# Performance work log

Measured on AMD Instinct MI355X. Metric: run time of the kernel, lower is better.

## Reference

```python
import jax, jax.numpy as jnp
import numpy as np

LAMBDA_ENERGY = 0.1
LAMBDA_COV = 0.005
TWO_PI = 2.0 * np.pi
EPS = 1e-12


def setup_inputs() -> dict:
    key = jax.random.key(0)
    k1, k2, k3, k4 = jax.random.split(key, 4)
    B, T, C, D, K, F = 32, 1024, 8, 8, 8, 64
    x = jax.random.normal(k1, (B, T, C, F), dtype=jnp.float32)
    x_hat = jax.random.normal(k2, (B, T, C, F), dtype=jnp.float32)
    z = jax.random.normal(k3, (B, T, C, D), dtype=jnp.float32)
    # gamma is a mixture-responsibility tensor (softmax output in DAGMM)
    gamma = jax.nn.softmax(jax.random.uniform(k4, (B, T, C, K), dtype=jnp.float32) * 4.0, axis=-1)
    return {"x": x, "x_hat": x_hat, "z": z, "gamma": gamma}


def _gmm_energy(z, gamma):
    # z: [B,T,C,D], gamma: [B,T,C,K]
    N = gamma.shape[0] * gamma.shape[1] * gamma.shape[2]
    gsum = jnp.sum(gamma, axis=(0, 1, 2))                      # [K]
    phi = gsum / N                                             # [K]
    mu = jnp.einsum('btck,btcd->kd', gamma, z) / gsum[:, None]  # [K,D]
    z_mu = z[..., None, :] - mu                                # [B,T,C,K,D]
    cov = jnp.einsum('btck,btcki,btckj->kij', gamma, z_mu, z_mu) / gsum[:, None, None]  # [K,D,D]

    D = cov.shape[-1]
    cov_k = cov + EPS * jnp.eye(D, dtype=cov.dtype)            # [K,D,D]
    cov_inv = jnp.linalg.inv(cov_k)                            # batched small-matrix inverse
    L = jnp.linalg.cholesky(TWO_PI * cov_k)                    # [K,D,D]
    det_cov = jnp.prod(jnp.diagonal(L, axis1=-2, axis2=-1), axis=-1)  # [K], = sqrt(det(2*pi*cov))
    cov_diag = jnp.sum(1.0 / jnp.diagonal(cov_k, axis1=-2, axis2=-1))

    # quadratic form per sample/component: [B,T,C,K]
    quad = jnp.einsum('btcki,kij,btckj->btck', z_mu, cov_inv, z_mu)
    E = jnp.exp(-0.5 * quad)
    E_z = -jnp.log(jnp.sum(phi * E / jnp.sqrt(det_cov), axis=-1) + EPS)
    return jnp.mean(E_z), cov_diag


def reference(x, x_hat, z, gamma):
    reconst_loss = jnp.mean((x_hat - x) ** 2)
    sample_energy, cov_diag = _gmm_energy(z, gamma)
    return reconst_loss + LAMBDA_ENERGY * sample_energy + LAMBDA_COV * cov_diag
```

## Files before the change

kernel.cpp:

```cpp
#include <hip/hip_runtime.h>
#include <math.h>

#define WS_RED   0
#define WS_EN    2048
#define WS_MU    3072
#define WS_CINV  3136
#define WS_COEF  3648
#define WS_CD    3656
#define WS_STATP 4096

static constexpr int NSAMP = 32 * 1024 * 8;
static constexpr int NX4   = NSAMP * 64 / 4;
static constexpr int RE_BLOCKS   = 2048;
static constexpr int STAT_BLOCKS = 256;
static constexpr int EN_BLOCKS   = 1024;
static constexpr float EPSF = 1e-12f;

__device__ inline float wave_reduce_sum(float v) {
    #pragma unroll
    for (int m = 1; m < 64; m <<= 1) v += __shfl_xor(v, m, 64);
    return v;
}
__device__ inline double wave_reduce_sum_d(double v) {
    #pragma unroll
    for (int m = 1; m < 64; m <<= 1) v += __shfl_xor(v, m, 64);
    return v;
}

__global__ __launch_bounds__(256) void krecon(const float4* __restrict__ x,
                                              const float4* __restrict__ xh,
                                              float* __restrict__ ws) {
    __shared__ float lds[4];
    const int t = blockIdx.x * 256 + threadIdx.x;

    float4 xa[8], xb[8];
    #pragma unroll
    for (int i = 0; i < 8; ++i) xa[i] = x[t + i * (RE_BLOCKS * 256)];
    #pragma unroll
    for (int i = 0; i < 8; ++i) xb[i] = xh[t + i * (RE_BLOCKS * 256)];

    float a0 = 0.f, a1 = 0.f, a2 = 0.f, a3 = 0.f;
    #pragma unroll
    for (int i = 0; i < 8; ++i) {
        float d0 = xb[i].x - xa[i].x;
        float d1 = xb[i].y - xa[i].y;
        float d2 = xb[i].z - xa[i].z;
        float d3 = xb[i].w - xa[i].w;
        a0 = fmaf(d0, d0, a0);
        a1 = fmaf(d1, d1, a1);
        a2 = fmaf(d2, d2, a2);
        a3 = fmaf(d3, d3, a3);
    }
    float acc = (a0 + a1) + (a2 + a3);

    acc = wave_reduce_sum(acc);
    int w = threadIdx.x >> 6;
    if ((threadIdx.x & 63) == 0) lds[w] = acc;
    __syncthreads();
    if (threadIdx.x == 0)
        ws[WS_RED + blockIdx.x] = lds[0] + lds[1] + lds[2] + lds[3];
}

__global__ __launch_bounds__(256) void kstats(const float4* __restrict__ z4,
                                              const float* __restrict__ gamma,
                                              float* __restrict__ ws) {
    __shared__ float lds[4][360];
    float acc[45];
    #pragma unroll
    for (int i = 0; i < 45; ++i) acc[i] = 0.f;

    const int k    = threadIdx.x & 7;
    const int grp  = (blockIdx.x << 5) | (threadIdx.x >> 3);
    constexpr int NGRP  = STAT_BLOCKS << 5;
    constexpr int ITERS = NSAMP / NGRP;

    for (int it = 0; it < ITERS; it += 4) {
        float4 za[4], zb[4];
        float gg[4];
        #pragma unroll
        for (int u = 0; u < 4; ++u) {
            int n = grp + (it + u) * NGRP;
            za[u] = z4[n * 2];
            zb[u] = z4[n * 2 + 1];
            gg[u] = gamma[n * 8 + k];
        }
        #pragma unroll
        for (int u = 0; u < 4; ++u) {
            float zv[8] = {za[u].x, za[u].y, za[u].z, za[u].w,
                           zb[u].x, zb[u].y, zb[u].z, zb[u].w};
            float g = gg[u];
            acc[0] += g;
            float gz[8];
            #pragma unroll
            for (int i = 0; i < 8; ++i) { gz[i] = g * zv[i]; acc[1 + i] += gz[i]; }
            #pragma unroll
            for (int i = 0; i < 8; ++i) {
                #pragma unroll
                for (int j = 0; j < 8; ++j) {
                    if (j <= i)
                        acc[9 + (i * (i + 1)) / 2 + j] =
                            fmaf(gz[i], zv[j], acc[9 + (i * (i + 1)) / 2 + j]);
                }
            }
        }
    }

    #pragma unroll
    for (int i = 0; i < 45; ++i) {
        float v = acc[i];
        v += __shfl_xor(v, 8, 64);
        v += __shfl_xor(v, 16, 64);
        v += __shfl_xor(v, 32, 64);
        acc[i] = v;
    }
    int lane = threadIdx.x & 63, w = threadIdx.x >> 6;
    if (lane < 8) {
        #pragma unroll
        for (int i = 0; i < 45; ++i) lds[w][lane * 45 + i] = acc[i];
    }
    __syncthreads();
    for (int v = threadIdx.x; v < 360; v += 256) {
        ws[WS_STATP + blockIdx.x * 360 + v] =
            lds[0][v] + lds[1][v] + lds[2][v] + lds[3][v];
    }
}

__global__ void kfinalize(float* __restrict__ ws) {
    __shared__ double sstat[360];
    int v = threadIdx.x;
    if (v < 360) {
        const float* p = &ws[WS_STATP + v];
        double s0 = 0.0, s1 = 0.0, s2 = 0.0, s3 = 0.0;
        #pragma unroll 4
        for (int b = 0; b < STAT_BLOCKS; b += 4) {
            s0 += (double)p[(b + 0) * 360];
            s1 += (double)p[(b + 1) * 360];
            s2 += (double)p[(b + 2) * 360];
            s3 += (double)p[(b + 3) * 360];
        }
        sstat[v] = (s0 + s1) + (s2 + s3);
    }
    __syncthreads();

    int k = threadIdx.x;
    if (k < 8) {
        const double* st = &sstat[k * 45];
        double g = st[0];
        double mu[8];
        for (int d = 0; d < 8; ++d) mu[d] = st[1 + d] / g;
        double A[8][8];
        {
            int t = 0;
            for (int i = 0; i < 8; ++i)
                for (int j = 0; j <= i; ++j) {
                    double val = st[9 + t] / g - mu[i] * mu[j];
                    A[i][j] = val; A[j][i] = val; ++t;
                }
        }
        for (int d = 0; d < 8; ++d) A[d][d] += (double)EPSF;

        double cd = 0.0;
        for (int d = 0; d < 8; ++d) cd += 1.0 / A[d][d];
        ws[WS_CD + k] = (float)cd;

        double L[8][8] = {};
        for (int i = 0; i < 8; ++i) {
            for (int j = 0; j <= i; ++j) {
                double s = A[i][j];
                for (int p = 0; p < j; ++p) s -= L[i][p] * L[j][p];
                if (i == j) L[i][i] = sqrt(s);
                else        L[i][j] = s / L[j][j];
            }
        }
        double M[8][8] = {};
        for (int i = 0; i < 8; ++i) {
            M[i][i] = 1.0 / L[i][i];
            for (int j = 0; j < i; ++j) {
                double s = 0.0;
                for (int p = j; p < i; ++p) s -= L[i][p] * M[p][j];
                M[i][j] = s / L[i][i];
            }
        }
        for (int i = 0; i < 8; ++i)
            for (int j = 0; j < 8; ++j) {
                double s = 0.0;
                int p0 = i > j ? i : j;
                for (int p = p0; p < 8; ++p) s += M[p][i] * M[p][j];
                ws[WS_CINV + k * 64 + i * 8 + j] = (float)s;
            }

        double det = 1.0;
        for (int d = 0; d < 8; ++d) det *= L[d][d];
        double c = 2.0 * M_PI;
        det *= c * c * c * c;
        double phi = g / (double)NSAMP;
        ws[WS_COEF + k] = (float)(phi / sqrt(det));
        for (int d = 0; d < 8; ++d) ws[WS_MU + k * 8 + d] = (float)mu[d];
    }
}

__global__ __launch_bounds__(256, 4) void kenergy(const float4* __restrict__ z4,
                                                  float* __restrict__ ws) {
    __shared__ float smu[64], scinv[512], scoef[8];
    __shared__ float lds[4];
    for (int i = threadIdx.x; i < 64; i += 256) smu[i] = ws[WS_MU + i];
    for (int i = threadIdx.x; i < 512; i += 256) scinv[i] = ws[WS_CINV + i];
    if (threadIdx.x < 8) scoef[threadIdx.x] = ws[WS_COEF + threadIdx.x];
    __syncthreads();

    const int n = blockIdx.x * 256 + threadIdx.x;
    float4 a = z4[n * 2], b = z4[n * 2 + 1];
    float zv[8] = {a.x, a.y, a.z, a.w, b.x, b.y, b.z, b.w};
    float sacc = 0.f;

    #pragma unroll 1
    for (int k = 0; k < 8; ++k) {
        float dv[8];
        #pragma unroll
        for (int i = 0; i < 8; ++i) dv[i] = zv[i] - smu[k * 8 + i];
        float quad = 0.f;
        #pragma unroll
        for (int i = 0; i < 8; ++i) {
            float4 c0 = *(const float4*)&scinv[k * 64 + i * 8];
            float4 c1 = *(const float4*)&scinv[k * 64 + i * 8 + 4];
            float r;
            r = c0.x * dv[0];
            r = fmaf(c0.y, dv[1], r);
            r = fmaf(c0.z, dv[2], r);
            r = fmaf(c0.w, dv[3], r);
            r = fmaf(c1.x, dv[4], r);
            r = fmaf(c1.y, dv[5], r);
            r = fmaf(c1.z, dv[6], r);
            r = fmaf(c1.w, dv[7], r);
            quad = fmaf(dv[i], r, quad);
        }
        sacc = fmaf(scoef[k], __expf(-0.5f * quad), sacc);
    }

    float acc = -__logf(sacc + EPSF);

    acc = wave_reduce_sum(acc);
    int w = threadIdx.x >> 6;
    if ((threadIdx.x & 63) == 0) lds[w] = acc;
    __syncthreads();
    if (threadIdx.x == 0)
        ws[WS_EN + blockIdx.x] = lds[0] + lds[1] + lds[2] + lds[3];
}

__global__ void kfinal(const float* __restrict__ ws, float* __restrict__ out) {
    __shared__ double ldsR[4], ldsE[4];
    double accR = 0.0, accE = 0.0;
    #pragma unroll 4
    for (int i = threadIdx.x; i < RE_BLOCKS; i += 256) accR += (double)ws[WS_RED + i];
    #pragma unroll 4
    for (int i = threadIdx.x; i < EN_BLOCKS; i += 256) accE += (double)ws[WS_EN + i];
    accR = wave_reduce_sum_d(accR);
    accE = wave_reduce_sum_d(accE);
    int w = threadIdx.x >> 6;
    if ((threadIdx.x & 63) == 0) { ldsR[w] = accR; ldsE[w] = accE; }
    __syncthreads();
    if (threadIdx.x == 0) {
        double R = ldsR[0] + ldsR[1] + ldsR[2] + ldsR[3];
        double E = ldsE[0] + ldsE[1] + ldsE[2] + ldsE[3];
        double cd = 0.0;
        for (int k = 0; k < 8; ++k) cd += (double)ws[WS_CD + k];
        double loss = R / ((double)NSAMP * 64.0)
                    + 0.1 * (E / (double)NSAMP)
                    + 0.005 * cd;
        out[0] = (float)loss;
    }
}

extern "C" void kernel_launch(void* const* d_in, const int* in_sizes, int n_in,
                              void* d_out, int out_size, void* d_ws, size_t ws_size,
                              hipStream_t stream) {
    const float* x     = (const float*)d_in[0];
    const float* xh    = (const float*)d_in[1];
    const float* z     = (const float*)d_in[2];
    const float* gamma = (const float*)d_in[3];
    float* ws = (float*)d_ws;

    krecon<<<RE_BLOCKS, 256, 0, stream>>>((const float4*)x, (const float4*)xh, ws);
    kstats<<<STAT_BLOCKS, 256, 0, stream>>>((const float4*)z, gamma, ws);
    kfinalize<<<1, 512, 0, stream>>>(ws);
    kenergy<<<EN_BLOCKS, 256, 0, stream>>>((const float4*)z, ws);
    kfinal<<<1, 256, 0, stream>>>(ws, (float*)d_out);
}
```

Before: 199.8 us.

## Fuse all stages into one persistent kernel with software grid barriers

Replaces the five kernel launches with a single persistent kernel of 1024 blocks that uses atomic-counter grid barriers to sequence reconstruction/stats, GMM parameter finalization, energy, and the final reduction. The reconstruction work is rebalanced so that the stats blocks take a smaller slice and the other blocks take more, which lets the stats pass overlap with the bandwidth-heavy reconstruction. The intent is to remove launch gaps and idle tails between stages. In exchange it relies on all 1024 blocks being co-resident (4 blocks per CU at 256 threads), adds spin-wait barrier cost and a memset, and leaves most of the grid idle while block 0 finalizes.

```diff
diff --git a/kernel.cpp b/kernel.cpp
--- a/kernel.cpp
+++ b/kernel.cpp
@@ -1,19 +1,20 @@
 #include <hip/hip_runtime.h>
 #include <math.h>
 
-#define WS_RED   0
-#define WS_EN    2048
-#define WS_MU    3072
-#define WS_CINV  3136
-#define WS_COEF  3648
-#define WS_CD    3656
+#define TPB   256
+#define GRID  1024
+#define SBLK  256
+
+#define WS_RED   64
+#define WS_EN    1088
+#define WS_MU    2112
+#define WS_CINV  2176
+#define WS_COEF  2688
+#define WS_CD    2696
 #define WS_STATP 4096
 
-static constexpr int NSAMP = 32 * 1024 * 8;
-static constexpr int NX4   = NSAMP * 64 / 4;
-static constexpr int RE_BLOCKS   = 2048;
-static constexpr int STAT_BLOCKS = 256;
-static constexpr int EN_BLOCKS   = 1024;
+static constexpr int NSAMP = 262144;
+static constexpr int NX4   = 4194304;
 static constexpr float EPSF = 1e-12f;
 
 __device__ inline float wave_reduce_sum(float v) {
@@ -27,247 +28,266 @@
     return v;
 }
 
-__global__ __launch_bounds__(256) void krecon(const float4* __restrict__ x,
-                                              const float4* __restrict__ xh,
-                                              float* __restrict__ ws) {
-    __shared__ float lds[4];
-    const int t = blockIdx.x * 256 + threadIdx.x;
-
-    float4 xa[8], xb[8];
-    #pragma unroll
-    for (int i = 0; i < 8; ++i) xa[i] = x[t + i * (RE_BLOCKS * 256)];
-    #pragma unroll
-    for (int i = 0; i < 8; ++i) xb[i] = xh[t + i * (RE_BLOCKS * 256)];
-
-    float a0 = 0.f, a1 = 0.f, a2 = 0.f, a3 = 0.f;
-    #pragma unroll
-    for (int i = 0; i < 8; ++i) {
-        float d0 = xb[i].x - xa[i].x;
-        float d1 = xb[i].y - xa[i].y;
-        float d2 = xb[i].z - xa[i].z;
-        float d3 = xb[i].w - xa[i].w;
-        a0 = fmaf(d0, d0, a0);
-        a1 = fmaf(d1, d1, a1);
-        a2 = fmaf(d2, d2, a2);
-        a3 = fmaf(d3, d3, a3);
-    }
-    float acc = (a0 + a1) + (a2 + a3);
-
-    acc = wave_reduce_sum(acc);
-    int w = threadIdx.x >> 6;
-    if ((threadIdx.x & 63) == 0) lds[w] = acc;
+__device__ inline void grid_barrier(unsigned* cnt, unsigned target) {
     __syncthreads();
-    if (threadIdx.x == 0)
-        ws[WS_RED + blockIdx.x] = lds[0] + lds[1] + lds[2] + lds[3];
-}
-
-__global__ __launch_bounds__(256) void kstats(const float4* __restrict__ z4,
-                                              const float* __restrict__ gamma,
-                                              float* __restrict__ ws) {
-    __shared__ float lds[4][360];
-    float acc[45];
-    #pragma unroll
-    for (int i = 0; i < 45; ++i) acc[i] = 0.f;
-
-    const int k    = threadIdx.x & 7;
-    const int grp  = (blockIdx.x << 5) | (threadIdx.x >> 3);
-    constexpr int NGRP  = STAT_BLOCKS << 5;
-    constexpr int ITERS = NSAMP / NGRP;
-
-    for (int it = 0; it < ITERS; it += 4) {
-        float4 za[4], zb[4];
-        float gg[4];
-        #pragma unroll
-        for (int u = 0; u < 4; ++u) {
-            int n = grp + (it + u) * NGRP;
-            za[u] = z4[n * 2];
-            zb[u] = z4[n * 2 + 1];
-            gg[u] = gamma[n * 8 + k];
-        }
-        #pragma unroll
-        for (int u = 0; u < 4; ++u) {
-            float zv[8] = {za[u].x, za[u].y, za[u].z, za[u].w,
-                           zb[u].x, zb[u].y, zb[u].z, zb[u].w};
-            float g = gg[u];
-            acc[0] += g;
-            float gz[8];
-            #pragma unroll
-            for (int i = 0; i < 8; ++i) { gz[i] = g * zv[i]; acc[1 + i] += gz[i]; }
-            #pragma unroll
-            for (int i = 0; i < 8; ++i) {
+    if (threadIdx.x == 0) {
+        __threadfence();
+        atomicAdd(cnt, 1u);
+        while (__hip_atomic_load(cnt, __ATOMIC_ACQUIRE,
+                                 __HIP_MEMORY_SCOPE_AGENT) < target)
+            __builtin_amdgcn_s_sleep(8);
+        __threadfence();
+    }
+    __syncthreads();
+}
+
+__global__ __launch_bounds__(TPB, 4) void kmega(const float4* __restrict__ x,
+                                                const float4* __restrict__ xh,
+                                                const float4* __restrict__ z4,
+                                                const float* __restrict__ gamma,
+                                                float* __restrict__ ws,
+                                                float* __restrict__ out) {
+    __shared__ float  sred[4];
+    __shared__ float  slds[4][360];
+    __shared__ double sstat[360];
+    __shared__ double schol[8][192];
+    __shared__ float  smu[64], scinv[512], scoef[8];
+    __shared__ double dred[4], dren[4];
+
+    unsigned* cnt = (unsigned*)ws;
+    const int b = blockIdx.x, tid = threadIdx.x;
+
+    float racc = 0.f;
+    if (b < SBLK) {
+        const int base = b * 1024 + tid;
+        float4 xa[4], xb[4];
+        #pragma unroll
+        for (int i = 0; i < 4; ++i) xa[i] = x[base + i * 256];
+        #pragma unroll
+        for (int i = 0; i < 4; ++i) xb[i] = xh[base + i * 256];
+        #pragma unroll
+        for (int i = 0; i < 4; ++i) {
+            float d0 = xb[i].x - xa[i].x, d1 = xb[i].y - xa[i].y;
+            float d2 = xb[i].z - xa[i].z, d3 = xb[i].w - xa[i].w;
+            racc = fmaf(d0, d0, racc); racc = fmaf(d1, d1, racc);
+            racc = fmaf(d2, d2, racc); racc = fmaf(d3, d3, racc);
+        }
+    } else {
+        const int base = SBLK * 1024 + (b - SBLK) * 5120 + tid;
+        #pragma unroll 1
+        for (int bt = 0; bt < 5; ++bt) {
+            float4 xa[4], xb[4];
+            #pragma unroll
+            for (int i = 0; i < 4; ++i) xa[i] = x[base + (bt * 4 + i) * 256];
+            #pragma unroll
+            for (int i = 0; i < 4; ++i) xb[i] = xh[base + (bt * 4 + i) * 256];
+            #pragma unroll
+            for (int i = 0; i < 4; ++i) {
+                float d0 = xb[i].x - xa[i].x, d1 = xb[i].y - xa[i].y;
+                float d2 = xb[i].z - xa[i].z, d3 = xb[i].w - xa[i].w;
+                racc = fmaf(d0, d0, racc); racc = fmaf(d1, d1, racc);
+                racc = fmaf(d2, d2, racc); racc = fmaf(d3, d3, racc);
+            }
+        }
+    }
+    {
+        float v = wave_reduce_sum(racc);
+        int w = tid >> 6;
+        if ((tid & 63) == 0) sred[w] = v;
+        __syncthreads();
+        if (tid == 0) ws[WS_RED + b] = sred[0] + sred[1] + sred[2] + sred[3];
+    }
+
+    if (b < SBLK) {
+        float acc[45];
+        #pragma unroll
+        for (int i = 0; i < 45; ++i) acc[i] = 0.f;
+        const int k = tid & 7;
+        const int sg = tid >> 3;
+        for (int it = 0; it < 32; it += 4) {
+            float4 za[4], zb[4]; float gg[4];
+            #pragma unroll
+            for (int u = 0; u < 4; ++u) {
+                int n = b * 1024 + (it + u) * 32 + sg;
+                za[u] = z4[n * 2]; zb[u] = z4[n * 2 + 1];
+                gg[u] = gamma[n * 8 + k];
+            }
+            #pragma unroll
+            for (int u = 0; u < 4; ++u) {
+                float zv[8] = {za[u].x, za[u].y, za[u].z, za[u].w,
+                               zb[u].x, zb[u].y, zb[u].z, zb[u].w};
+                float g = gg[u];
+                acc[0] += g;
+                float gz[8];
                 #pragma unroll
-                for (int j = 0; j < 8; ++j) {
-                    if (j <= i)
-                        acc[9 + (i * (i + 1)) / 2 + j] =
-                            fmaf(gz[i], zv[j], acc[9 + (i * (i + 1)) / 2 + j]);
+                for (int i = 0; i < 8; ++i) { gz[i] = g * zv[i]; acc[1 + i] += gz[i]; }
+                #pragma unroll
+                for (int i = 0; i < 8; ++i) {
+                    #pragma unroll
+                    for (int j = 0; j < 8; ++j) {
+                        if (j <= i)
+                            acc[9 + (i * (i + 1)) / 2 + j] =
+                                fmaf(gz[i], zv[j], acc[9 + (i * (i + 1)) / 2 + j]);
+                    }
                 }
             }
         }
-    }
-
-    #pragma unroll
-    for (int i = 0; i < 45; ++i) {
-        float v = acc[i];
-        v += __shfl_xor(v, 8, 64);
-        v += __shfl_xor(v, 16, 64);
-        v += __shfl_xor(v, 32, 64);
-        acc[i] = v;
-    }
-    int lane = threadIdx.x & 63, w = threadIdx.x >> 6;
-    if (lane < 8) {
-        #pragma unroll
-        for (int i = 0; i < 45; ++i) lds[w][lane * 45 + i] = acc[i];
-    }
-    __syncthreads();
-    for (int v = threadIdx.x; v < 360; v += 256) {
-        ws[WS_STATP + blockIdx.x * 360 + v] =
-            lds[0][v] + lds[1][v] + lds[2][v] + lds[3][v];
-    }
-}
-
-__global__ void kfinalize(float* __restrict__ ws) {
-    __shared__ double sstat[360];
-    int v = threadIdx.x;
-    if (v < 360) {
-        const float* p = &ws[WS_STATP + v];
-        double s0 = 0.0, s1 = 0.0, s2 = 0.0, s3 = 0.0;
-        #pragma unroll 4
-        for (int b = 0; b < STAT_BLOCKS; b += 4) {
-            s0 += (double)p[(b + 0) * 360];
-            s1 += (double)p[(b + 1) * 360];
-            s2 += (double)p[(b + 2) * 360];
-            s3 += (double)p[(b + 3) * 360];
-        }
-        sstat[v] = (s0 + s1) + (s2 + s3);
-    }
-    __syncthreads();
-
-    int k = threadIdx.x;
-    if (k < 8) {
-        const double* st = &sstat[k * 45];
-        double g = st[0];
-        double mu[8];
-        for (int d = 0; d < 8; ++d) mu[d] = st[1 + d] / g;
-        double A[8][8];
-        {
-            int t = 0;
+        #pragma unroll
+        for (int i = 0; i < 45; ++i) {
+            float v = acc[i];
+            v += __shfl_xor(v, 8, 64);
+            v += __shfl_xor(v, 16, 64);
+            v += __shfl_xor(v, 32, 64);
+            acc[i] = v;
+        }
+        int lane = tid & 63, w = tid >> 6;
+        if (lane < 8) {
+            #pragma unroll
+            for (int i = 0; i < 45; ++i) slds[w][lane * 45 + i] = acc[i];
+        }
+        __syncthreads();
+        for (int v = tid; v < 360; v += TPB)
+            ws[WS_STATP + v * 256 + b] =
+                slds[0][v] + slds[1][v] + slds[2][v] + slds[3][v];
+    }
+
+    grid_barrier(cnt + 0, GRID);
+
+    if (b == 0) {
+        for (int v = tid; v < 360; v += TPB) {
+            const float4* p = (const float4*)&ws[WS_STATP + v * 256];
+            double s0 = 0, s1 = 0, s2 = 0, s3 = 0;
+            #pragma unroll 4
+            for (int q = 0; q < 64; q += 4) {
+                float4 a0 = p[q], a1 = p[q + 1], a2 = p[q + 2], a3 = p[q + 3];
+                s0 += (double)a0.x + (double)a0.y + (double)a0.z + (double)a0.w;
+                s1 += (double)a1.x + (double)a1.y + (double)a1.z + (double)a1.w;
+                s2 += (double)a2.x + (double)a2.y + (double)a2.z + (double)a2.w;
+                s3 += (double)a3.x + (double)a3.y + (double)a3.z + (double)a3.w;
+            }
+            sstat[v] = (s0 + s1) + (s2 + s3);
+        }
+        __syncthreads();
+        if (tid < 8) {
+            const int k = tid;
+            double* A = &schol[k][0];
+            double* L = &schol[k][64];
+            double* M = &schol[k][128];
+            const double* st = &sstat[k * 45];
+            double g = st[0];
+            double mu[8];
+            for (int d = 0; d < 8; ++d) mu[d] = st[1 + d] / g;
+            {
+                int t = 0;
+                for (int i = 0; i < 8; ++i)
+                    for (int j = 0; j <= i; ++j) {
+                        double v = st[9 + t] / g - mu[i] * mu[j];
+                        A[i * 8 + j] = v; A[j * 8 + i] = v; ++t;
+                    }
+            }
+            for (int d = 0; d < 8; ++d) A[d * 8 + d] += (double)EPSF;
+
+            double cd = 0.0;
+            for (int d = 0; d < 8; ++d) cd += 1.0 / A[d * 8 + d];
+            ws[WS_CD + k] = (float)cd;
+
             for (int i = 0; i < 8; ++i)
                 for (int j = 0; j <= i; ++j) {
-                    double val = st[9 + t] / g - mu[i] * mu[j];
-                    A[i][j] = val; A[j][i] = val; ++t;
+                    double s = A[i * 8 + j];
+                    for (int p = 0; p < j; ++p) s -= L[i * 8 + p] * L[j * 8 + p];
+                    if (i == j) L[i * 8 + i] = sqrt(s);
+                    else        L[i * 8 + j] = s / L[j * 8 + j];
                 }
-        }
-        for (int d = 0; d < 8; ++d) A[d][d] += (double)EPSF;
-
-        double cd = 0.0;
-        for (int d = 0; d < 8; ++d) cd += 1.0 / A[d][d];
-        ws[WS_CD + k] = (float)cd;
-
-        double L[8][8] = {};
-        for (int i = 0; i < 8; ++i) {
-            for (int j = 0; j <= i; ++j) {
-                double s = A[i][j];
-                for (int p = 0; p < j; ++p) s -= L[i][p] * L[j][p];
-                if (i == j) L[i][i] = sqrt(s);
-                else        L[i][j] = s / L[j][j];
-            }
-        }
-        double M[8][8] = {};
-        for (int i = 0; i < 8; ++i) {
-            M[i][i] = 1.0 / L[i][i];
-            for (int j = 0; j < i; ++j) {
-                double s = 0.0;
-                for (int p = j; p < i; ++p) s -= L[i][p] * M[p][j];
-                M[i][j] = s / L[i][i];
-            }
-        }
-        for (int i = 0; i < 8; ++i)
-            for (int j = 0; j < 8; ++j) {
-                double s = 0.0;
-                int p0 = i > j ? i : j;
-                for (int p = p0; p < 8; ++p) s += M[p][i] * M[p][j];
-                ws[WS_CINV + k * 64 + i * 8 + j] = (float)s;
-            }
-
-        double det = 1.0;
-        for (int d = 0; d < 8; ++d) det *= L[d][d];
-        double c = 2.0 * M_PI;
-        det *= c * c * c * c;
-        double phi = g / (double)NSAMP;
-        ws[WS_COEF + k] = (float)(phi / sqrt(det));
-        for (int d = 0; d < 8; ++d) ws[WS_MU + k * 8 + d] = (float)mu[d];
-    }
-}
-
-__global__ __launch_bounds__(256, 4) void kenergy(const float4* __restrict__ z4,
-                                                  float* __restrict__ ws) {
-    __shared__ float smu[64], scinv[512], scoef[8];
-    __shared__ float lds[4];
-    for (int i = threadIdx.x; i < 64; i += 256) smu[i] = ws[WS_MU + i];
-    for (int i = threadIdx.x; i < 512; i += 256) scinv[i] = ws[WS_CINV + i];
-    if (threadIdx.x < 8) scoef[threadIdx.x] = ws[WS_COEF + threadIdx.x];
+            for (int i = 0; i < 8; ++i) {
+                M[i * 8 + i] = 1.0 / L[i * 8 + i];
+                for (int j = 0; j < i; ++j) {
+                    double s = 0.0;
+                    for (int p = j; p < i; ++p) s -= L[i * 8 + p] * M[p * 8 + j];
+                    M[i * 8 + j] = s / L[i * 8 + i];
+                }
+            }
+            for (int i = 0; i < 8; ++i)
+                for (int j = 0; j < 8; ++j) {
+                    double s = 0.0;
+                    int p0 = i > j ? i : j;
+                    for (int p = p0; p < 8; ++p) s += M[p * 8 + i] * M[p * 8 + j];
+                    ws[WS_CINV + k * 64 + i * 8 + j] = (float)s;
+                }
+            double det = 1.0;
+            for (int d = 0; d < 8; ++d) det *= L[d * 8 + d];
+            double c = 2.0 * M_PI;
+            det *= c * c * c * c;
+            ws[WS_COEF + k] = (float)((g / (double)NSAMP) / sqrt(det));
+            for (int d = 0; d < 8; ++d) ws[WS_MU + k * 8 + d] = (float)mu[d];
+        }
+    }
+
+    grid_barrier(cnt + 1, GRID);
+
+    for (int i = tid; i < 64;  i += TPB) smu[i]   = ws[WS_MU + i];
+    for (int i = tid; i < 512; i += TPB) scinv[i] = ws[WS_CINV + i];
+    if (tid < 8) scoef[tid] = ws[WS_COEF + tid];
     __syncthreads();
 
-    const int n = blockIdx.x * 256 + threadIdx.x;
-    float4 a = z4[n * 2], b = z4[n * 2 + 1];
-    float zv[8] = {a.x, a.y, a.z, a.w, b.x, b.y, b.z, b.w};
-    float sacc = 0.f;
-
-    #pragma unroll 1
-    for (int k = 0; k < 8; ++k) {
-        float dv[8];
-        #pragma unroll
-        for (int i = 0; i < 8; ++i) dv[i] = zv[i] - smu[k * 8 + i];
-        float quad = 0.f;
-        #pragma unroll
-        for (int i = 0; i < 8; ++i) {
-            float4 c0 = *(const float4*)&scinv[k * 64 + i * 8];
-            float4 c1 = *(const float4*)&scinv[k * 64 + i * 8 + 4];
-            float r;
-            r = c0.x * dv[0];
-            r = fmaf(c0.y, dv[1], r);
-            r = fmaf(c0.z, dv[2], r);
-            r = fmaf(c0.w, dv[3], r);
-            r = fmaf(c1.x, dv[4], r);
-            r = fmaf(c1.y, dv[5], r);
-            r = fmaf(c1.z, dv[6], r);
-            r = fmaf(c1.w, dv[7], r);
-            quad = fmaf(dv[i], r, quad);
-        }
-        sacc = fmaf(scoef[k], __expf(-0.5f * quad), sacc);
-    }
-
-    float acc = -__logf(sacc + EPSF);
-
-    acc = wave_reduce_sum(acc);
-    int w = threadIdx.x >> 6;
-    if ((threadIdx.x & 63) == 0) lds[w] = acc;
-    __syncthreads();
-    if (threadIdx.x == 0)
-        ws[WS_EN + blockIdx.x] = lds[0] + lds[1] + lds[2] + lds[3];
-}
-
-__global__ void kfinal(const float* __restrict__ ws, float* __restrict__ out) {
-    __shared__ double ldsR[4], ldsE[4];
-    double accR = 0.0, accE = 0.0;
-    #pragma unroll 4
-    for (int i = threadIdx.x; i < RE_BLOCKS; i += 256) accR += (double)ws[WS_RED + i];
-    #pragma unroll 4
-    for (int i = threadIdx.x; i < EN_BLOCKS; i += 256) accE += (double)ws[WS_EN + i];
-    accR = wave_reduce_sum_d(accR);
-    accE = wave_reduce_sum_d(accE);
-    int w = threadIdx.x >> 6;
-    if ((threadIdx.x & 63) == 0) { ldsR[w] = accR; ldsE[w] = accE; }
-    __syncthreads();
-    if (threadIdx.x == 0) {
-        double R = ldsR[0] + ldsR[1] + ldsR[2] + ldsR[3];
-        double E = ldsE[0] + ldsE[1] + ldsE[2] + ldsE[3];
-        double cd = 0.0;
-        for (int k = 0; k < 8; ++k) cd += (double)ws[WS_CD + k];
-        double loss = R / ((double)NSAMP * 64.0)
-                    + 0.1 * (E / (double)NSAMP)
-                    + 0.005 * cd;
-        out[0] = (float)loss;
+    {
+        const int n = b * 256 + tid;
+        float4 a = z4[n * 2], bb = z4[n * 2 + 1];
+        float zv[8] = {a.x, a.y, a.z, a.w, bb.x, bb.y, bb.z, bb.w};
+        float sacc = 0.f;
+        #pragma unroll 1
+        for (int k = 0; k < 8; ++k) {
+            float dv[8];
+            #pragma unroll
+            for (int i = 0; i < 8; ++i) dv[i] = zv[i] - smu[k * 8 + i];
+            float quad = 0.f;
+            #pragma unroll
+            for (int i = 0; i < 8; ++i) {
+                float4 c0 = *(const float4*)&scinv[k * 64 + i * 8];
+                float4 c1 = *(const float4*)&scinv[k * 64 + i * 8 + 4];
+                float r;
+                r = c0.x * dv[0];
+                r = fmaf(c0.y, dv[1], r);
+                r = fmaf(c0.z, dv[2], r);
+                r = fmaf(c0.w, dv[3], r);
+                r = fmaf(c1.x, dv[4], r);
+                r = fmaf(c1.y, dv[5], r);
+                r = fmaf(c1.z, dv[6], r);
+                r = fmaf(c1.w, dv[7], r);
+                quad = fmaf(dv[i], r, quad);
+            }
+            sacc = fmaf(scoef[k], __expf(-0.5f * quad), sacc);
+        }
+        float e = -__logf(sacc + EPSF);
+        float v = wave_reduce_sum(e);
+        __syncthreads();
+        int w = tid >> 6;
+        if ((tid & 63) == 0) sred[w] = v;
+        __syncthreads();
+        if (tid == 0) ws[WS_EN + b] = sred[0] + sred[1] + sred[2] + sred[3];
+    }
+
+    grid_barrier(cnt + 2, GRID);
+
+    if (b == 0) {
+        double accR = 0.0, accE = 0.0;
+        #pragma unroll 4
+        for (int i = tid; i < GRID; i += TPB) accR += (double)ws[WS_RED + i];
+        #pragma unroll 4
+        for (int i = tid; i < GRID; i += TPB) accE += (double)ws[WS_EN + i];
+        accR = wave_reduce_sum_d(accR);
+        accE = wave_reduce_sum_d(accE);
+        int w = tid >> 6;
+        if ((tid & 63) == 0) { dred[w] = accR; dren[w] = accE; }
+        __syncthreads();
+        if (tid == 0) {
+            double R = dred[0] + dred[1] + dred[2] + dred[3];
+            double E = dren[0] + dren[1] + dren[2] + dren[3];
+            double cd = 0.0;
+            for (int k = 0; k < 8; ++k) cd += (double)ws[WS_CD + k];
+            out[0] = (float)(R / ((double)NSAMP * 64.0)
+                           + 0.1 * (E / (double)NSAMP)
+                           + 0.005 * cd);
+        }
     }
 }
 
@@ -280,9 +300,7 @@
     const float* gamma = (const float*)d_in[3];
     float* ws = (float*)d_ws;
 
-    krecon<<<RE_BLOCKS, 256, 0, stream>>>((const float4*)x, (const float4*)xh, ws);
-    kstats<<<STAT_BLOCKS, 256, 0, stream>>>((const float4*)z, gamma, ws);
-    kfinalize<<<1, 512, 0, stream>>>(ws);
-    kenergy<<<EN_BLOCKS, 256, 0, stream>>>((const float4*)z, ws);
-    kfinal<<<1, 256, 0, stream>>>(ws, (float*)d_out);
-}
+    hipMemsetAsync(ws, 0, 64, stream);
+    kmega<<<GRID, TPB, 0, stream>>>((const float4*)x, (const float4*)xh,
+                                    (const float4*)z, gamma, ws, (float*)d_out);
+}
```

Measured after the change: 706.8 us. +253.8%, slower.
